# Kernel optimization log

Measured on AMD Instinct MI355X. Metric: run time of the kernel, lower is better.

Reference implementation:

```python
import jax, jax.numpy as jnp
from jax import lax
import numpy as np

B, T, F = 64, 128, 16
H = 512
S = 2  # num_seg; SEG_DICT['2'] = [8, 6], seg_cumsum = [2, 10, 16]


def timestep_embedding(t, dim, max_period=10000.0):
    half = dim // 2
    freqs = jnp.exp(-jnp.log(max_period) * jnp.arange(half, dtype=jnp.float32) / half)
    args = t[:, None] * freqs  # [N, half]
    return jnp.concatenate([jnp.cos(args), jnp.sin(args)], axis=-1)  # [N, dim]


def setup_inputs() -> dict:
    key = jax.random.key(0)
    ks = jax.random.split(key, 16)
    sc = lambda *sh: 1.0 / np.sqrt(sh[-1])
    inp = {
        'x': jax.random.normal(ks[0], (B, T, F), dtype=jnp.float32),
        'lengths': jax.random.randint(ks[1], (B,), 1, T + 1),
        'h0': jax.random.uniform(ks[2], (B, H), dtype=jnp.float32),
        'c0': jax.random.uniform(ks[3], (B, H), dtype=jnp.float32),
        'W_is0': jax.random.normal(ks[4], (H, 8), dtype=jnp.float32) * sc(8),
        'b_is0': jax.random.normal(ks[5], (H,), dtype=jnp.float32) * 0.01,
        'W_is1': jax.random.normal(ks[6], (H, 6), dtype=jnp.float32) * sc(6),
        'b_is1': jax.random.normal(ks[7], (H,), dtype=jnp.float32) * 0.01,
        'W_ih': jax.random.normal(ks[8], (4 * H, 3 * H), dtype=jnp.float32) * sc(3 * H),
        'W_hh': jax.random.normal(ks[9], (4 * H, H), dtype=jnp.float32) * sc(H),
        'b_ih': jax.random.normal(ks[10], (4 * H,), dtype=jnp.float32) * 0.01,
        'b_hh': jax.random.normal(ks[11], (4 * H,), dtype=jnp.float32) * 0.01,
        'W_o': jax.random.normal(ks[12], (F - 2, S * H), dtype=jnp.float32) * sc(S * H),
        'b_o': jax.random.normal(ks[13], (F - 2,), dtype=jnp.float32) * 0.01,
    }
    return inp


def reference(x, lengths, h0, c0, W_is0, b_is0, W_is1, b_is1,
              W_ih, W_hh, b_ih, b_hh, W_o, b_o):
    b, t, f = x.shape
    h = h0.shape[1]
    xf = x.reshape(-1, f)  # [B*T, F]

    # timestep embeddings from the two time columns (learning_type='diff')
    tc = timestep_embedding(xf[:, 0], h)
    tp = timestep_embedding(xf[:, 1], h)
    t_emb = jnp.concatenate([tc, tp], axis=-1)  # [B*T, 2H]

    # per-segment input linears (segments = cols 2:10 and 10:16)
    e0 = xf[:, 2:10] @ W_is0.T + b_is0
    e1 = xf[:, 10:16] @ W_is1.T + b_is1
    e0 = jnp.concatenate([e0, t_emb], axis=-1)[:, None, :]  # [B*T, 1, 3H]
    e1 = jnp.concatenate([e1, t_emb], axis=-1)[:, None, :]
    # faithful to torch: concat on dim=1 then reshape(batch, num_seg, seq_len, -1)
    embs = jnp.concatenate([e0, e1], axis=1).reshape(b, S, t, 3 * h)

    def cell(carry, xt):
        hh, cc = carry
        gates = xt @ W_ih.T + b_ih + hh @ W_hh.T + b_hh
        i, fg, g, o = jnp.split(gates, 4, axis=-1)  # torch LSTMCell order i,f,g,o
        cc = jax.nn.sigmoid(fg) * cc + jax.nn.sigmoid(i) * jnp.tanh(g)
        hh = jax.nn.sigmoid(o) * jnp.tanh(cc)
        return (hh, cc), hh

    hs = []
    for s in range(S):  # shared cell weights across segments (same nn.LSTMCell object)
        xs = jnp.swapaxes(embs[:, s], 0, 1)  # [T, B, 3H]
        _, h_seq = lax.scan(cell, (h0, c0), xs)  # [T, B, H]
        hs.append(jnp.swapaxes(h_seq, 0, 1))  # [B, T, H]
    hidden_states = jnp.stack(hs, axis=-2)  # [B, T, S, H]; dropout rate 0 -> identity

    idx = lengths - 1  # final valid timestep per sequence
    hfin = hidden_states[jnp.arange(b), idx].reshape(b, S * h)  # [B, S*H]
    out = jax.nn.sigmoid(hfin @ W_o.T + b_o)  # mlp_o: Linear + Sigmoid
    return out
```

## Files before the change

kernel.cpp:

```cpp
#include <hip/hip_runtime.h>
#include <hip/hip_bf16.h>
#include <stdint.h>


typedef __attribute__((ext_vector_type(8))) short bf16x8_t;
typedef __attribute__((ext_vector_type(4))) float f32x4_t;

#define SENT 0xAAAAAAAAu

#define OFF_G      0u
#define OFF_TEMB   33554432u
#define OFF_HH     50331648u
#define OFF_WHH    67239936u
#define OFF_WMID   69337088u
#define OFF_WC0    73531392u
#define OFF_WC1    73596928u
#define OFF_BC     73662464u
#define OFF_HFIN   73678848u
#define OFF_GFLAG  73940992u

__device__ __forceinline__ float bf2f(uint16_t u){
  union { uint32_t i; float f; } v; v.i = ((uint32_t)u) << 16; return v.f;
}
__device__ __forceinline__ uint16_t f2b(float f){
  union { float f; uint32_t i; } v; v.f = f;
  uint32_t r = v.i + 0x7fffu + ((v.i >> 16) & 1u);
  return (uint16_t)(r >> 16);
}
__device__ __forceinline__ float sigm(float x){ return 1.0f/(1.0f + __expf(-x)); }
__device__ __forceinline__ float tanh_(float x){
  float xc = fminf(fmaxf(x, -15.f), 15.f);
  float t = __expf(2.f*xc);
  return (t - 1.f)/(t + 1.f);
}
__device__ __forceinline__ void gl_lds16(const void* g, void* l){
  __builtin_amdgcn_global_load_lds(
      (const __attribute__((address_space(1))) void*)g,
      (__attribute__((address_space(3))) void*)l, 16, 0, 0);
}

__global__ void prepAll(const float* __restrict__ x,
                        const float* __restrict__ W_ih, const float* __restrict__ W_hh,
                        const float* __restrict__ W_is0, const float* __restrict__ b_is0,
                        const float* __restrict__ W_is1, const float* __restrict__ b_is1,
                        const float* __restrict__ b_ih, const float* __restrict__ b_hh,
                        const float* __restrict__ h0,
                        uint16_t* __restrict__ whh_b, uint16_t* __restrict__ wmid_b,
                        float* __restrict__ wc0, float* __restrict__ wc1,
                        float* __restrict__ bc,
                        uint16_t* __restrict__ temb, uint16_t* __restrict__ h_hist,
                        uint32_t* __restrict__ gflag){
  const int bid = blockIdx.x, tid = threadIdx.x;
  if (bid < 2048){
    const int n = bid;
    __shared__ float wrow[512];
    __shared__ float red[16][17];
    wrow[tid]       = W_ih[(size_t)n*1536 + tid];
    wrow[tid + 256] = W_ih[(size_t)n*1536 + 256 + tid];
    for (int j = tid; j < 1024; j += 256)
      wmid_b[(size_t)n*1024 + j] = f2b(W_ih[(size_t)n*1536 + 512 + j]);
    for (int k = tid; k < 512; k += 256)
      whh_b[(size_t)n*512 + k] = f2b(W_hh[(size_t)n*512 + k]);
    __syncthreads();
    {
      const int d = tid >> 4, jp = tid & 15;
      float s = 0.f;
      const int kk0 = jp*32;
      if (d < 8){
        for (int k = kk0; k < kk0 + 32; ++k) s += wrow[k]*W_is0[k*8 + d];
      } else if (d < 14){
        int c = d - 8;
        for (int k = kk0; k < kk0 + 32; ++k) s += wrow[k]*W_is1[k*6 + c];
      } else if (d == 14){
        for (int k = kk0; k < kk0 + 32; ++k) s += wrow[k]*b_is0[k];
      } else {
        for (int k = kk0; k < kk0 + 32; ++k) s += wrow[k]*b_is1[k];
      }
      red[d][jp] = s;
    }
    __syncthreads();
    if (tid < 16){
      float tot = 0.f;
      #pragma unroll
      for (int i = 0; i < 16; ++i) tot += red[tid][i];
      if (tid < 8)        wc0[n*8 + tid] = tot;
      else if (tid < 14)  wc1[n*8 + (tid - 8)] = tot;
      else if (tid == 14) bc[n]        = b_ih[n] + b_hh[n] + tot;
      else                bc[2048 + n] = b_ih[n] + b_hh[n] + tot;
    } else if (tid == 16){
      wc1[n*8 + 6] = 0.f; wc1[n*8 + 7] = 0.f;
    }
  } else if (bid < 10240){
    const int rid = bid - 2048;
    const int k = tid;
    float x0 = x[(size_t)rid*16 + 0], x1 = x[(size_t)rid*16 + 1];
    float f = __expf((float)k * (-9.210340371976184f/256.f));
    float a0 = x0*f, a1 = x1*f;
    size_t base = (size_t)rid*1024;
    temb[base + k]        = f2b(__cosf(a0));
    temb[base + 256 + k]  = f2b(__sinf(a0));
    temb[base + 512 + k]  = f2b(__cosf(a1));
    temb[base + 768 + k]  = f2b(__sinf(a1));
  } else if (bid < 10368){
    int i = (bid - 10240)*256 + tid;
    uint32_t* hh = (uint32_t*)h_hist;
    int e    = i*2;
    int rrcg = e >> 9;
    int rr   = rrcg >> 4, cg = rrcg & 15;
    int rm   = e & 511;
    int row  = rm >> 5, u = rm & 31;
    int b    = (rr*16 + row) & 63;
    int unit = cg*32 + u;
    uint32_t lo = f2b(h0[(size_t)b*512 + unit]);
    uint32_t hi = f2b(h0[(size_t)b*512 + unit + 1]);
    uint32_t wd = lo | (hi << 16);
    if (wd == SENT) wd ^= 1u;
    hh[i] = wd;
    if (i < 1024) gflag[i] = 0u;
  } else {
    uint32_t* hh = (uint32_t*)h_hist;
    size_t w0 = 32768u + ((size_t)(bid - 10368)*256 + tid)*8;
    uint4 s4 = make_uint4(SENT, SENT, SENT, SENT);
    *(uint4*)&hh[w0]     = s4;
    *(uint4*)&hh[w0 + 4] = s4;
  }
}

__launch_bounds__(256)
__global__ void fusedk(const float* __restrict__ x, const float* __restrict__ c0,
                       const int* __restrict__ lengths,
                       const uint16_t* __restrict__ whh_b, const uint16_t* __restrict__ temb,
                       const uint16_t* __restrict__ wmid,
                       const float* __restrict__ wc0, const float* __restrict__ wc1,
                       const float* __restrict__ bc,
                       uint16_t* __restrict__ G, uint16_t* __restrict__ h_hist,
                       uint32_t* __restrict__ gflag, float* __restrict__ hfin){
  __shared__ __align__(16) uint16_t smem_u[17664];
  const int tid = threadIdx.x;
  const int bid = blockIdx.x;
  const int w = tid >> 6, lane = tid & 63;
  const int q = lane >> 4, ln = lane & 15;

  if (bid >= 128){
    const int gb = bid - 128;
    const int idx = gb >> 4;
    const int mt = (idx & 1) ? (idx >> 1) : (32 + (idx >> 1));
    const int n0 = (gb & 15)*128;
    uint16_t* Al = smem_u;
    uint16_t* Bl = smem_u + 8192;
    const int wm = w >> 1, wn = w & 1;
    const int srow_l = lane >> 3;
    const int scol = (((lane & 7) ^ srow_l)) * 8;

    f32x4_t acc[4][4];
    #pragma unroll
    for (int a = 0; a < 4; ++a)
      #pragma unroll
      for (int b2 = 0; b2 < 4; ++b2) acc[a][b2] = (f32x4_t){0.f,0.f,0.f,0.f};

    for (int kb = 0; kb < 16; ++kb){
      #pragma unroll
      for (int i = 0; i < 4; ++i){
        int row0 = w*32 + i*8;
        int lrow = row0 + srow_l;
        int bA = lrow & 63, ntmA = mt*2 + (lrow >> 6);
        gl_lds16(temb + (size_t)(bA*128 + ntmA)*1024 + kb*64 + scol, &Al[row0*64]);
        gl_lds16(wmid + (size_t)(n0 + lrow)*1024 + kb*64 + scol, &Bl[row0*64]);
      }
      __syncthreads();
      #pragma unroll
      for (int kc = 0; kc < 2; ++kc){
        const int sl = ((((kc << 2) | q) ^ (ln & 7)) << 3);
        bf16x8_t af[4], bf[4];
        #pragma unroll
        for (int mt_i = 0; mt_i < 4; ++mt_i)
          af[mt_i] = *(const bf16x8_t*)&Al[(wm*64 + mt_i*16 + ln)*64 + sl];
        #pragma unroll
        for (int nt = 0; nt < 4; ++nt)
          bf[nt] = *(const bf16x8_t*)&Bl[(wn*64 + nt*16 + ln)*64 + sl];
        #pragma unroll
        for (int mt_i = 0; mt_i < 4; ++mt_i)
          #pragma unroll
          for (int nt = 0; nt < 4; ++nt)
            acc[mt_i][nt] = __builtin_amdgcn_mfma_f32_16x16x32_bf16(af[mt_i], bf[nt], acc[mt_i][nt], 0, 0, 0);
      }
      __syncthreads();
    }
    #pragma unroll
    for (int mt_i = 0; mt_i < 4; ++mt_i)
      #pragma unroll
      for (int nt = 0; nt < 4; ++nt)
        #pragma unroll
        for (int r = 0; r < 4; ++r){
          int Mr = wm*64 + mt_i*16 + q*4 + r;
          int Nc = wn*64 + nt*16 + ln;
          smem_u[Mr*132 + Nc] = f2b(acc[mt_i][nt][r]);
        }
    __syncthreads();
    {
      const int erow = tid >> 1, eh = tid & 1;
      const unsigned long long* lsrc = (const unsigned long long*)&smem_u[erow*132 + eh*64];
      unsigned long long* gdst = (unsigned long long*)
          (G + (size_t)(mt*128 + erow)*2048 + n0 + eh*64);
      #pragma unroll
      for (int i2 = 0; i2 < 16; ++i2)
        __hip_atomic_store(&gdst[i2], lsrc[i2], __ATOMIC_RELAXED, __HIP_MEMORY_SCOPE_AGENT);
    }
    __syncthreads();
    if (tid == 0)
      __hip_atomic_store(&gflag[mt*16 + (gb & 15)], 1u,
                         __ATOMIC_RELEASE, __HIP_MEMORY_SCOPE_AGENT);
    return;
  }

  #define HL(b,r,c) smem_u[(((b)*16 + (r))*552) + (c)]
  const int rr = bid & 7;
  const int g  = bid >> 3;
  const int k0 = g*32;
  const int sp = rr >> 2;
  const int u8 = ln & 7, gh = ln >> 3;
  const int unit = k0 + w*8 + u8;
  const int gl0 = gh*512 + unit;
  const int gl1 = (2 + gh)*512 + unit;
  const int LVL = 65536;

  bf16x8_t barr0[16], barr1[16];
  #pragma unroll
  for (int kc = 0; kc < 16; ++kc){
    barr0[kc] = *(const bf16x8_t*)(whh_b + (size_t)gl0*512 + kc*32 + q*8);
    barr1[kc] = *(const bf16x8_t*)(whh_b + (size_t)gl1*512 + kc*32 + q*8);
  }
  bf16x8_t e0f[2], e1f[2];
  #pragma unroll
  for (int nsI = 0; nsI < 2; ++nsI){
    bf16x8_t v0 = {0,0,0,0,0,0,0,0}, v1 = {0,0,0,0,0,0,0,0};
    if (q == 0){
      const float* wcs = nsI ? wc1 : wc0;
      #pragma unroll
      for (int jj = 0; jj < 8; ++jj){
        ((uint16_t*)&v0)[jj] = f2b(wcs[gl0*8 + jj]);
        ((uint16_t*)&v1)[jj] = f2b(wcs[gl1*8 + jj]);
      }
    }
    e0f[nsI] = v0; e1f[nsI] = v1;
  }
  float bc0v[2] = { bc[gl0], bc[2048 + gl0] };
  float bc1v[2] = { bc[gl1], bc[2048 + gl1] };

  int   bmr[4], lenr[4];
  float cst[4];
  #pragma unroll
  for (int r = 0; r < 4; ++r){
    int row = rr*16 + q*4 + r;
    bmr[r]  = row & 63;
    lenr[r] = lengths[bmr[r]];
    cst[r]  = c0[(size_t)bmr[r]*512 + unit];
  }

  const int prow = lane >> 2;
  const int pcol = (lane & 3)*8;
  const int xm = tid >> 3, xc = tid & 7;
  const int xb = (rr*16 + xm) & 63;
  const size_t stb = ((size_t)rr*8192 + g*512);

  for (int idx2 = tid; idx2 < 2*16*32; idx2 += 256)
    HL(idx2 >> 9, (idx2 >> 5) & 15, 520 + (idx2 & 31)) = 0;

  uint32_t fl[4];
  {
    const uint32_t* gf0 = gflag + (sp*32)*16 + (g >> 2);
    #pragma unroll
    for (int j = 0; j < 4; ++j)
      fl[j] = __hip_atomic_load(&gf0[j*4], __ATOMIC_RELAXED, __HIP_MEMORY_SCOPE_AGENT);
  }

  for (int t = 0; t < 128; ++t){
    const int qidx = sp*128 + t;
    const int ntm = qidx >> 1;
    const int ns  = qidx & 1;
    const int buf = t & 1;

    if ((t & 3) == 0){
      const int mt = qidx >> 2;
      bool ok = (fl[0] != 0u) & (fl[1] != 0u) & (fl[2] != 0u) & (fl[3] != 0u);
      if (!ok){
        const uint32_t* gf = gflag + mt*16 + (g >> 2);
        while (true){
          ok = true;
          #pragma unroll
          for (int j = 0; j < 4; ++j){
            uint32_t v = __hip_atomic_load(&gf[j*4], __ATOMIC_RELAXED, __HIP_MEMORY_SCOPE_AGENT);
            ok &= (v != 0u);
          }
          if (ok) break;
          __builtin_amdgcn_s_sleep(1);
        }
      }
      if (t < 124){
        const uint32_t* gfn = gflag + (mt + 1)*16 + (g >> 2);
        #pragma unroll
        for (int j = 0; j < 4; ++j)
          fl[j] = __hip_atomic_load(&gfn[j*4], __ATOMIC_RELAXED, __HIP_MEMORY_SCOPE_AGENT);
      }
    }

    uint16_t g0r[4], g1r[4];
    #pragma unroll
    for (int r = 0; r < 4; ++r){
      size_t grow = (size_t)(ntm*64 + bmr[r])*2048;
      g0r[r] = G[grow + gl0];
      g1r[r] = G[grow + gl1];
    }
    float xv = 0.f;
    if (tid < 128){
      if (ns == 0)      xv = x[(size_t)(xb*128 + ntm)*16 + 2 + xc];
      else if (xc < 6)  xv = x[(size_t)(xb*128 + ntm)*16 + 10 + xc];
    }

    {
      const unsigned long long* lvl = (const unsigned long long*)h_hist
                                      + (((size_t)t*LVL + (size_t)rr*8192) >> 2);
      unsigned long long hv[4][2];
      while (true){
        bool ok = true;
        #pragma unroll
        for (int i = 0; i < 4; ++i){
          const unsigned long long* p = lvl + ((size_t)(w*4 + i)*128 + prow*8 + (pcol >> 2));
          hv[i][0] = __hip_atomic_load(&p[0], __ATOMIC_RELAXED, __HIP_MEMORY_SCOPE_AGENT);
          hv[i][1] = __hip_atomic_load(&p[1], __ATOMIC_RELAXED, __HIP_MEMORY_SCOPE_AGENT);
          ok &= ((uint32_t)hv[i][0] != SENT) & ((uint32_t)(hv[i][0] >> 32) != SENT)
              & ((uint32_t)hv[i][1] != SENT) & ((uint32_t)(hv[i][1] >> 32) != SENT);
        }
        if (__all(ok)) break;
        __builtin_amdgcn_s_sleep(1);
      }
      #pragma unroll
      for (int i = 0; i < 4; ++i){
        int reg = w*4 + i;
        *(unsigned long long*)&HL(buf, prow, reg*32 + pcol)     = hv[i][0];
        *(unsigned long long*)&HL(buf, prow, reg*32 + pcol + 4) = hv[i][1];
      }
    }
    if (tid < 128) HL(buf, xm, 512 + xc) = f2b(xv);
    __syncthreads();

    f32x4_t acc0, acc1;
    {
      float b0 = ns ? bc0v[1] : bc0v[0];
      float b1 = ns ? bc1v[1] : bc1v[0];
      #pragma unroll
      for (int r = 0; r < 4; ++r){ acc0[r] = bf2f(g0r[r]) + b0; acc1[r] = bf2f(g1r[r]) + b1; }
    }
    #pragma unroll
    for (int kc = 0; kc < 16; ++kc){
      bf16x8_t a = *(const bf16x8_t*)&HL(buf, ln, kc*32 + q*8);
      acc0 = __builtin_amdgcn_mfma_f32_16x16x32_bf16(a, barr0[kc], acc0, 0, 0, 0);
      acc1 = __builtin_amdgcn_mfma_f32_16x16x32_bf16(a, barr1[kc], acc1, 0, 0, 0);
    }
    {
      bf16x8_t a = *(const bf16x8_t*)&HL(buf, ln, 512 + q*8);
      acc0 = __builtin_amdgcn_mfma_f32_16x16x32_bf16(a, ns ? e0f[1] : e0f[0], acc0, 0, 0, 0);
      acc1 = __builtin_amdgcn_mfma_f32_16x16x32_bf16(a, ns ? e1f[1] : e1f[0], acc1, 0, 0, 0);
    }

    float pf[4], po[4];
    #pragma unroll
    for (int r = 0; r < 4; ++r){
      pf[r] = __shfl_xor(acc0[r], 8);
      po[r] = __shfl_xor(acc1[r], 8);
    }
    if (ln < 8){
      uint32_t hb[4]; float hF[4];
      #pragma unroll
      for (int r = 0; r < 4; ++r){
        float ig = acc0[r], fg = pf[r], gg = acc1[r], og = po[r];
        cst[r] = sigm(fg)*cst[r] + sigm(ig)*tanh_(gg);
        float h = sigm(og)*tanh_(cst[r]);
        hF[r] = h; hb[r] = (uint32_t)f2b(h);
      }
      #pragma unroll
      for (int r = 0; r < 4; ++r){
        uint32_t ph = (uint32_t)__shfl_xor((int)hb[r], 1);
        uint32_t packed = hb[r] | (ph << 16);
        if (packed == SENT) packed ^= 1u;
        uint32_t hi = (uint32_t)__shfl_xor((int)packed, 2);
        if ((ln & 3) == 0){
          unsigned long long v = (unsigned long long)packed | ((unsigned long long)hi << 32);
          unsigned long long* hp = (unsigned long long*)h_hist
              + (((size_t)(t+1)*LVL + stb + (size_t)(q*4 + r)*32 + w*8 + u8) >> 2);
          __hip_atomic_store(hp, v, __ATOMIC_RELAXED, __HIP_MEMORY_SCOPE_AGENT);
        }
        if (t == lenr[r] - 1)
          hfin[(size_t)bmr[r]*1024 + sp*512 + unit] = hF[r];
      }
    }
  }
  #undef HL
}

__global__ void outk(const float* __restrict__ hfin, const float* __restrict__ W_o,
                     const float* __restrict__ b_o, float* __restrict__ out){
  __shared__ float hl[1024];
  __shared__ float red[16][17];
  const int b = blockIdx.x, tid = threadIdx.x;
  #pragma unroll
  for (int i = 0; i < 4; ++i) hl[tid + i*256] = hfin[(size_t)b*1024 + tid + i*256];
  __syncthreads();
  const int o = tid >> 4, j0 = tid & 15;
  float s = 0.f;
  if (o < 14){
    for (int j = j0; j < 1024; j += 16) s += hl[j]*W_o[(size_t)o*1024 + j];
  }
  red[o][j0] = s;
  __syncthreads();
  if (tid < 14){
    float tot = b_o[tid];
    #pragma unroll
    for (int i = 0; i < 16; ++i) tot += red[tid][i];
    out[b*14 + tid] = 1.0f/(1.0f + __expf(-tot));
  }
}

extern "C" void kernel_launch(void* const* d_in, const int* in_sizes, int n_in,
                              void* d_out, int out_size, void* d_ws, size_t ws_size,
                              hipStream_t stream){
  const float* x     = (const float*)d_in[0];
  const int*   lens  = (const int*)  d_in[1];
  const float* h0    = (const float*)d_in[2];
  const float* c0    = (const float*)d_in[3];
  const float* W_is0 = (const float*)d_in[4];
  const float* b_is0 = (const float*)d_in[5];
  const float* W_is1 = (const float*)d_in[6];
  const float* b_is1 = (const float*)d_in[7];
  const float* W_ih  = (const float*)d_in[8];
  const float* W_hh  = (const float*)d_in[9];
  const float* b_ih  = (const float*)d_in[10];
  const float* b_hh  = (const float*)d_in[11];
  const float* W_o   = (const float*)d_in[12];
  const float* b_o   = (const float*)d_in[13];
  float* out = (float*)d_out;

  char* ws = (char*)d_ws;
  uint16_t* G      = (uint16_t*)(ws + OFF_G);
  uint16_t* temb   = (uint16_t*)(ws + OFF_TEMB);
  uint16_t* h_hist = (uint16_t*)(ws + OFF_HH);
  uint16_t* whh_b  = (uint16_t*)(ws + OFF_WHH);
  uint16_t* wmid_b = (uint16_t*)(ws + OFF_WMID);
  float* wc0  = (float*)(ws + OFF_WC0);
  float* wc1  = (float*)(ws + OFF_WC1);
  float* bc   = (float*)(ws + OFF_BC);
  float* hfin = (float*)(ws + OFF_HFIN);
  uint32_t* gflag = (uint32_t*)(ws + OFF_GFLAG);

  hipLaunchKernelGGL(prepAll, dim3(12416), dim3(256), 0, stream,
                     x, W_ih, W_hh, W_is0, b_is0, W_is1, b_is1, b_ih, b_hh, h0,
                     whh_b, wmid_b, wc0, wc1, bc, temb, h_hist, gflag);
  hipLaunchKernelGGL(fusedk, dim3(1152), dim3(256), 0, stream,
                     x, c0, lens, whh_b, temb, wmid_b, wc0, wc1, bc,
                     G, h_hist, gflag, hfin);
  hipLaunchKernelGGL(outk, dim3(64), dim3(256), 0, stream, hfin, W_o, b_o, out);
}
```

Measured before the change: 567.3 us.

## Use XCD-local volatile h exchange when recurrence group shares one XCD

```diff
diff --git a/kernel.cpp b/kernel.cpp
--- a/kernel.cpp
+++ b/kernel.cpp
@@ -18,6 +18,7 @@
 #define OFF_BC     73662464u
 #define OFF_HFIN   73678848u
 #define OFF_GFLAG  73940992u
+#define OFF_XCDT   73945088u
 
 __device__ __forceinline__ float bf2f(uint16_t u){
   union { uint32_t i; float f; } v; v.i = ((uint32_t)u) << 16; return v.f;
@@ -49,7 +50,7 @@
                         float* __restrict__ wc0, float* __restrict__ wc1,
                         float* __restrict__ bc,
                         uint16_t* __restrict__ temb, uint16_t* __restrict__ h_hist,
-                        uint32_t* __restrict__ gflag){
+                        uint32_t* __restrict__ gflag, uint32_t* __restrict__ xcdtab){
   const int bid = blockIdx.x, tid = threadIdx.x;
   if (bid < 2048){
     const int n = bid;
@@ -117,6 +118,7 @@
     if (wd == SENT) wd ^= 1u;
     hh[i] = wd;
     if (i < 1024) gflag[i] = 0u;
+    if (i < 128)  xcdtab[i] = 0xFFFFFFFFu;
   } else {
     uint32_t* hh = (uint32_t*)h_hist;
     size_t w0 = 32768u + ((size_t)(bid - 10368)*256 + tid)*8;
@@ -134,7 +136,8 @@
                        const float* __restrict__ wc0, const float* __restrict__ wc1,
                        const float* __restrict__ bc,
                        uint16_t* __restrict__ G, uint16_t* __restrict__ h_hist,
-                       uint32_t* __restrict__ gflag, float* __restrict__ hfin){
+                       uint32_t* __restrict__ gflag, uint32_t* __restrict__ xcdtab,
+                       float* __restrict__ hfin){
   __shared__ __align__(16) uint16_t smem_u[17664];
   const int tid = threadIdx.x;
   const int bid = blockIdx.x;
@@ -213,6 +216,7 @@
     return;
   }
 
+  __builtin_amdgcn_s_setprio(2);
   #define HL(b,r,c) smem_u[(((b)*16 + (r))*552) + (c)]
   const int rr = bid & 7;
   const int g  = bid >> 3;
@@ -265,6 +269,31 @@
 
   for (int idx2 = tid; idx2 < 2*16*32; idx2 += 256)
     HL(idx2 >> 9, (idx2 >> 5) & 15, 520 + (idx2 & 31)) = 0;
+
+  int fastv = 0;
+  {
+    uint32_t myxcd;
+    asm volatile("s_getreg_b32 %0, hwreg(HW_REG_XCC_ID)" : "=s"(myxcd));
+    if (tid == 0)
+      __hip_atomic_store(&xcdtab[bid], myxcd, __ATOMIC_RELAXED, __HIP_MEMORY_SCOPE_AGENT);
+    uint32_t pv = 0xFFFFFFFFu;
+    if (tid < 16){
+      const uint32_t* pp = &xcdtab[tid*8 + rr];
+      for (int it = 0; it < 20000; ++it){
+        pv = __hip_atomic_load(pp, __ATOMIC_RELAXED, __HIP_MEMORY_SCOPE_AGENT);
+        if (pv != 0xFFFFFFFFu) break;
+        __builtin_amdgcn_s_sleep(4);
+      }
+    }
+    bool ok = (tid >= 16) || (pv == myxcd);
+    if (tid < 64){
+      bool allok = __all(ok);
+      if (tid == 0) *(volatile int*)&smem_u[0] = allok ? 1 : 0;
+    }
+    __syncthreads();
+    fastv = *(volatile int*)&smem_u[0];
+    __syncthreads();
+  }
 
   uint32_t fl[4];
   {
@@ -323,13 +352,26 @@
       unsigned long long hv[4][2];
       while (true){
         bool ok = true;
-        #pragma unroll
-        for (int i = 0; i < 4; ++i){
-          const unsigned long long* p = lvl + ((size_t)(w*4 + i)*128 + prow*8 + (pcol >> 2));
-          hv[i][0] = __hip_atomic_load(&p[0], __ATOMIC_RELAXED, __HIP_MEMORY_SCOPE_AGENT);
-          hv[i][1] = __hip_atomic_load(&p[1], __ATOMIC_RELAXED, __HIP_MEMORY_SCOPE_AGENT);
-          ok &= ((uint32_t)hv[i][0] != SENT) & ((uint32_t)(hv[i][0] >> 32) != SENT)
-              & ((uint32_t)hv[i][1] != SENT) & ((uint32_t)(hv[i][1] >> 32) != SENT);
+        if (fastv){
+          #pragma unroll
+          for (int i = 0; i < 4; ++i){
+            const volatile unsigned long long* p =
+                (const volatile unsigned long long*)
+                (lvl + ((size_t)(w*4 + i)*128 + prow*8 + (pcol >> 2)));
+            hv[i][0] = p[0];
+            hv[i][1] = p[1];
+            ok &= ((uint32_t)hv[i][0] != SENT) & ((uint32_t)(hv[i][0] >> 32) != SENT)
+                & ((uint32_t)hv[i][1] != SENT) & ((uint32_t)(hv[i][1] >> 32) != SENT);
+          }
+        } else {
+          #pragma unroll
+          for (int i = 0; i < 4; ++i){
+            const unsigned long long* p = lvl + ((size_t)(w*4 + i)*128 + prow*8 + (pcol >> 2));
+            hv[i][0] = __hip_atomic_load(&p[0], __ATOMIC_RELAXED, __HIP_MEMORY_SCOPE_AGENT);
+            hv[i][1] = __hip_atomic_load(&p[1], __ATOMIC_RELAXED, __HIP_MEMORY_SCOPE_AGENT);
+            ok &= ((uint32_t)hv[i][0] != SENT) & ((uint32_t)(hv[i][0] >> 32) != SENT)
+                & ((uint32_t)hv[i][1] != SENT) & ((uint32_t)(hv[i][1] >> 32) != SENT);
+          }
         }
         if (__all(ok)) break;
         __builtin_amdgcn_s_sleep(1);
@@ -388,7 +430,8 @@
           unsigned long long v = (unsigned long long)packed | ((unsigned long long)hi << 32);
           unsigned long long* hp = (unsigned long long*)h_hist
               + (((size_t)(t+1)*LVL + stb + (size_t)(q*4 + r)*32 + w*8 + u8) >> 2);
-          __hip_atomic_store(hp, v, __ATOMIC_RELAXED, __HIP_MEMORY_SCOPE_AGENT);
+          if (fastv) *(volatile unsigned long long*)hp = v;
+          else __hip_atomic_store(hp, v, __ATOMIC_RELAXED, __HIP_MEMORY_SCOPE_AGENT);
         }
         if (t == lenr[r] - 1)
           hfin[(size_t)bmr[r]*1024 + sp*512 + unit] = hF[r];
@@ -451,12 +494,13 @@
   float* bc   = (float*)(ws + OFF_BC);
   float* hfin = (float*)(ws + OFF_HFIN);
   uint32_t* gflag = (uint32_t*)(ws + OFF_GFLAG);
+  uint32_t* xcdtab = (uint32_t*)(ws + OFF_XCDT);
 
   hipLaunchKernelGGL(prepAll, dim3(12416), dim3(256), 0, stream,
                      x, W_ih, W_hh, W_is0, b_is0, W_is1, b_is1, b_ih, b_hh, h0,
-                     whh_b, wmid_b, wc0, wc1, bc, temb, h_hist, gflag);
+                     whh_b, wmid_b, wc0, wc1, bc, temb, h_hist, gflag, xcdtab);
   hipLaunchKernelGGL(fusedk, dim3(1152), dim3(256), 0, stream,
                      x, c0, lens, whh_b, temb, wmid_b, wc0, wc1, bc,
-                     G, h_hist, gflag, hfin);
+                     G, h_hist, gflag, xcdtab, hfin);
   hipLaunchKernelGGL(outk, dim3(64), dim3(256), 0, stream, hfin, W_o, b_o, out);
 }
```

After: 874.6 us. +54.2%, slower.
